# Performance work log

Hardware: AMD Instinct MI355X
Metric: run time of the kernel (lower is better)

Reference implementation:

```python
import jax, jax.numpy as jnp
import numpy as np

K = 3          # kernel size
PAD = 1        # padding


def _conv2d(x, w, b):
    # plain 3x3 conv, stride 1, pad 1, NCHW / OIHW
    out = jax.lax.conv_general_dilated(
        x, w, window_strides=(1, 1), padding=((PAD, PAD), (PAD, PAD)),
        dimension_numbers=('NCHW', 'OIHW', 'NCHW'))
    return out + b[None, :, None, None]


def _deform_conv2d(x, offsets, w, b):
    # torchvision deform_conv2d semantics (stride=1, dilation=1, no mask)
    B, C, H, W = x.shape
    K2 = K * K
    off = offsets.reshape(B, K2, 2, H, W)
    dy, dx = off[:, :, 0], off[:, :, 1]              # [B,K2,H,W], (y,x) order
    ki, kj = jnp.meshgrid(jnp.arange(K), jnp.arange(K), indexing='ij')
    ki = ki.reshape(K2).astype(x.dtype)
    kj = kj.reshape(K2).astype(x.dtype)
    base_y = (jnp.arange(H, dtype=x.dtype)[None, :, None] - PAD + ki[:, None, None])  # [K2,H,1]
    base_x = (jnp.arange(W, dtype=x.dtype)[None, None, :] - PAD + kj[:, None, None])  # [K2,1,W]
    py = base_y[None] + dy                            # [B,K2,H,W] sampling rows
    px = base_x[None] + dx                            # [B,K2,H,W] sampling cols

    y0 = jnp.floor(py); x0 = jnp.floor(px)
    y1 = y0 + 1.0;      x1 = x0 + 1.0
    wy1 = py - y0; wy0 = 1.0 - wy1
    wx1 = px - x0; wx0 = 1.0 - wx1

    def corner(yc, xc, wgt):
        valid = ((yc >= 0) & (yc <= H - 1) & (xc >= 0) & (xc <= W - 1))
        iy = jnp.clip(yc, 0, H - 1).astype(jnp.int32)
        ix = jnp.clip(xc, 0, W - 1).astype(jnp.int32)
        # per-batch gather: x[b][:, iy[b], ix[b]] -> [C,K2,H,W]
        vals = jax.vmap(lambda xb, iyb, ixb: xb[:, iyb, ixb])(x, iy, ix)
        return vals * (wgt * valid.astype(x.dtype))[:, None]  # [B,C,K2,H,W]

    sampled = (corner(y0, x0, wy0 * wx0) + corner(y0, x1, wy0 * wx1)
               + corner(y1, x0, wy1 * wx0) + corner(y1, x1, wy1 * wx1))
    out = jnp.einsum('bckhw,ock->bohw', sampled, w.reshape(w.shape[0], C, K2))
    return out + b[None, :, None, None]


def setup_inputs() -> dict:
    key = jax.random.key(0)
    ks = jax.random.split(key, 6)
    B, C, O, H, W = 4, 256, 256, 64, 64
    x = jax.random.normal(ks[0], (B, C, H, W), dtype=jnp.float32)
    y = jax.random.normal(ks[1], (B, C, H, W), dtype=jnp.float32)
    # offset conv predicts 2*K*K offset channels; small init keeps offsets a few px
    offset_w = jax.random.normal(ks[2], (2 * K * K, C, K, K), dtype=jnp.float32) * 0.01
    offset_b = jax.random.normal(ks[3], (2 * K * K,), dtype=jnp.float32) * 0.01
    deform_w = jax.random.normal(ks[4], (O, C, K, K), dtype=jnp.float32) * (1.0 / np.sqrt(C * K * K))
    deform_b = jax.random.normal(ks[5], (O,), dtype=jnp.float32) * 0.01
    return {"x": x, "y": y, "offset_w": offset_w, "offset_b": offset_b,
            "deform_w": deform_w, "deform_b": deform_b}


def reference(x, y, offset_w, offset_b, deform_w, deform_b):
    offsets = _conv2d(y, offset_w, offset_b)          # [B, 2*K*K, H, W]
    return _deform_conv2d(x, offsets, deform_w, deform_b)
```

## Files before the change

kernel.cpp:

```cpp
#include <hip/hip_runtime.h>
#include <hip/hip_bf16.h>
#include <stdint.h>


typedef __bf16 bf16x8 __attribute__((ext_vector_type(8)));
typedef float  f32x4  __attribute__((ext_vector_type(4)));

__device__ __forceinline__ unsigned short f2bfu(float f) {
    union { float f; unsigned u; } v; v.f = f;
    return (unsigned short)((v.u + 0x8000u) >> 16);
}
__device__ __forceinline__ float lo16(unsigned u) {
    union { unsigned u; float f; } v; v.u = u << 16; return v.f;
}
__device__ __forceinline__ float hi16(unsigned u) {
    union { unsigned u; float f; } v; v.u = u & 0xFFFF0000u; return v.f;
}
__device__ __forceinline__ unsigned fbits(float f) {
    union { float f; unsigned u; } v; v.f = f; return v.u;
}
__device__ __forceinline__ unsigned blend2(unsigned u0, unsigned u1, unsigned u2, unsigned u3,
                                           float4 w) {
    float lo = w.x * lo16(u0) + w.y * lo16(u1) + w.z * lo16(u2) + w.w * lo16(u3);
    float hi = w.x * hi16(u0) + w.y * hi16(u1) + w.z * hi16(u2) + w.w * hi16(u3);
    unsigned rl = fbits(lo) + 0x8000u;
    unsigned rh = fbits(hi) + 0x8000u;
    return __builtin_amdgcn_perm(rh, rl, 0x07060302);
}

__global__ __launch_bounds__(256) void prep_kernel(
    const float* __restrict__ x, const float* __restrict__ y,
    const float* __restrict__ ow, const float* __restrict__ dw,
    unsigned short* __restrict__ xT, unsigned short* __restrict__ yT,
    unsigned short* __restrict__ Wp2, unsigned short* __restrict__ Bo)
{
    __shared__ float tile[64 * 69];
    int blk = blockIdx.x;
    int t = threadIdx.x;
    if (blk < 2048) {
        const float* src = x; unsigned short* dst = xT;
        if (blk >= 1024) { src = y; dst = yT; blk -= 1024; }
        int cq = blk & 3;
        int bh = blk >> 2;
        int w4 = t & 15, cl0 = t >> 4;
        const float* s = src + ((size_t)(bh >> 6) * 256 + cq * 64) * 4096 + (size_t)(bh & 63) * 64;
#pragma unroll
        for (int p = 0; p < 4; ++p) {
            int cl = p * 16 + cl0;
            float4 v = *(const float4*)&s[(size_t)cl * 4096 + w4 * 4];
            tile[(w4 * 4 + 0) * 69 + cl] = v.x;
            tile[(w4 * 4 + 1) * 69 + cl] = v.y;
            tile[(w4 * 4 + 2) * 69 + cl] = v.z;
            tile[(w4 * 4 + 3) * 69 + cl] = v.w;
        }
        __syncthreads();
        unsigned short* d = dst + (size_t)bh * 16384 + cq * 64;
#pragma unroll
        for (int p = 0; p < 4; ++p) {
            int w = p * 16 + cl0;
            float4 v = *(const float4*)&tile[w * 69 + w4 * 4];
            ushort4 r = make_ushort4(f2bfu(v.x), f2bfu(v.y), f2bfu(v.z), f2bfu(v.w));
            *(ushort4*)&d[w * 256 + w4 * 4] = r;
        }
    } else if (blk < 2336) {
        int tid = (blk - 2048) * 256 + t;
        int q8 = tid >> 8;
        int o  = tid & 255;
        int k0 = q8 * 8;
        int tap = k0 >> 8, c0 = k0 & 255;
        const float* s = dw + o * 2304 + c0 * 9 + tap;
        ushort4 r0 = make_ushort4(f2bfu(s[0]), f2bfu(s[9]), f2bfu(s[18]), f2bfu(s[27]));
        ushort4 r1 = make_ushort4(f2bfu(s[36]), f2bfu(s[45]), f2bfu(s[54]), f2bfu(s[63]));
        *(ushort4*)&Wp2[tid * 8 + 0] = r0;
        *(ushort4*)&Wp2[tid * 8 + 4] = r1;
    } else {
        int idx = (blk - 2336) * 256 + t;
        int j = idx & 7;
        int n = (idx >> 3) & 31;
        int lq = (idx >> 8) & 3;
        int kg = idx >> 10;
        int k = kg * 32 + lq * 8 + j;
        int tap = k >> 8, c = k & 255;
        float v = (n < 18) ? ow[n * 2304 + c * 9 + tap] : 0.f;
        Bo[idx] = f2bfu(v);
    }
}

__global__ __launch_bounds__(1024) void deform_kernel(
    const unsigned short* __restrict__ xT,
    const unsigned short* __restrict__ yT,
    const unsigned short* __restrict__ Wp2,
    const unsigned short* __restrict__ Bo,
    const float* __restrict__ ob,
    const float* __restrict__ db,
    float* __restrict__ out)
{
    __shared__ __align__(16) unsigned char smem[88064];
    unsigned short* Abuf0 = (unsigned short*)smem;
    unsigned short* Abuf1 = (unsigned short*)(smem + 32768);
    float*  red = (float*)smem;
    float*  epi = (float*)smem;
    float4* pw_lds = (float4*)(smem + 69632);
    int4*   pi_lds = (int4*)(smem + 69632 + 9216);

    int blk = blockIdx.x;
    int lb = (blk & 7) * 32 + (blk >> 3);
    int b = lb >> 6, h = lb & 63;
    int t = threadIdx.x;
    int wv = t >> 6, lane = t & 63;
    int ln = lane & 15, lq = lane >> 4;

    const unsigned short* xtb = xT + (size_t)b * (64 * 64 * 256);

    {
        int kq = wv >> 1, mh = wv & 1;
        f32x4 oacc[2][2];
#pragma unroll
        for (int m16 = 0; m16 < 2; ++m16)
#pragma unroll
            for (int nt = 0; nt < 2; ++nt)
                oacc[m16][nt] = (f32x4){0.f, 0.f, 0.f, 0.f};
        for (int u = kq * 9; u < kq * 9 + 9; ++u) {
            int tap = u >> 3, kc = u & 7;
            int ki = tap / 3, kj = tap - ki * 3;
            int hr = h + ki - 1;
            bf16x8 b0 = *(const bf16x8*)&Bo[(tap * 8 + kc) * 1024 + lq * 256 + ln * 8];
            bf16x8 b1 = *(const bf16x8*)&Bo[(tap * 8 + kc) * 1024 + lq * 256 + (16 + ln) * 8];
#pragma unroll
            for (int m16 = 0; m16 < 2; ++m16) {
                int wr = mh * 32 + m16 * 16 + ln + kj - 1;
                bf16x8 af = (bf16x8)(__bf16)0.0f;
                if (hr >= 0 && hr < 64 && wr >= 0 && wr < 64)
                    af = *(const bf16x8*)&yT[((size_t)(b * 64 + hr) * 64 + wr) * 256 + kc * 32 + lq * 8];
                oacc[m16][0] = __builtin_amdgcn_mfma_f32_16x16x32_bf16(af, b0, oacc[m16][0], 0, 0, 0);
                oacc[m16][1] = __builtin_amdgcn_mfma_f32_16x16x32_bf16(af, b1, oacc[m16][1], 0, 0, 0);
            }
        }
        float* rz = red + (size_t)(kq * 2 + mh) * 1056;
#pragma unroll
        for (int m16 = 0; m16 < 2; ++m16)
#pragma unroll
            for (int nt = 0; nt < 2; ++nt) {
                int o_l = nt * 16 + ln;
#pragma unroll
                for (int r = 0; r < 4; ++r)
                    rz[o_l * 33 + m16 * 16 + lq * 4 + r] = oacc[m16][nt][r];
            }
    }
    __syncthreads();
    if (t < 576) {
        int tap = t >> 6, pos = t & 63;
        int mh_p = pos >> 5, pl = pos & 31;
        float dy = ob[2 * tap], dx = ob[2 * tap + 1];
#pragma unroll
        for (int kq = 0; kq < 8; ++kq) {
            const float* rz = red + (size_t)(kq * 2 + mh_p) * 1056;
            dy += rz[(2 * tap) * 33 + pl];
            dx += rz[(2 * tap + 1) * 33 + pl];
        }
        int ki = tap / 3, kj = tap - ki * 3;
        float py = (float)(h - 1 + ki) + dy;
        float px = (float)(pos - 1 + kj) + dx;
        float y0 = floorf(py), x0 = floorf(px);
        float wy1 = py - y0, wx1 = px - x0;
        float wy0 = 1.f - wy1, wx0 = 1.f - wx1;
        float y1 = y0 + 1.f, x1 = x0 + 1.f;
        float vy0 = (y0 >= 0.f && y0 <= 63.f) ? 1.f : 0.f;
        float vy1 = (y1 >= 0.f && y1 <= 63.f) ? 1.f : 0.f;
        float vx0 = (x0 >= 0.f && x0 <= 63.f) ? 1.f : 0.f;
        float vx1 = (x1 >= 0.f && x1 <= 63.f) ? 1.f : 0.f;
        int iy0 = (int)fminf(fmaxf(y0, 0.f), 63.f);
        int iy1 = (int)fminf(fmaxf(y1, 0.f), 63.f);
        int ix0 = (int)fminf(fmaxf(x0, 0.f), 63.f);
        int ix1 = (int)fminf(fmaxf(x1, 0.f), 63.f);
        pw_lds[t] = make_float4(wy0 * wx0 * vy0 * vx0, wy0 * wx1 * vy0 * vx1,
                                wy1 * wx0 * vy1 * vx0, wy1 * wx1 * vy1 * vx1);
        pi_lds[t] = make_int4((iy0 * 64 + ix0) * 256, (iy0 * 64 + ix1) * 256,
                              (iy1 * 64 + ix0) * 256, (iy1 * 64 + ix1) * 256);
    }
    __syncthreads();

    int ns = wv & 7, kh = wv >> 3;

    f32x4 acc[4][2];
#pragma unroll
    for (int ms = 0; ms < 4; ++ms)
#pragma unroll
        for (int nt = 0; nt < 2; ++nt)
            acc[ms][nt] = (f32x4){0.f, 0.f, 0.f, 0.f};

    int gr = t & 31, c0 = gr * 8;
    uint4 ga[2][4]; float4 gw[2];
#pragma unroll
    for (int it = 0; it < 2; ++it) {
        int pos = (t >> 5) + it * 32;
        gw[it] = pw_lds[pos];
        int4 p = pi_lds[pos];
        ga[it][0] = *(const uint4*)&xtb[p.x + c0];
        ga[it][1] = *(const uint4*)&xtb[p.y + c0];
        ga[it][2] = *(const uint4*)&xtb[p.z + c0];
        ga[it][3] = *(const uint4*)&xtb[p.w + c0];
    }
#pragma unroll
    for (int it = 0; it < 2; ++it) {
        int pos = (t >> 5) + it * 32;
        uint4 res;
        res.x = blend2(ga[it][0].x, ga[it][1].x, ga[it][2].x, ga[it][3].x, gw[it]);
        res.y = blend2(ga[it][0].y, ga[it][1].y, ga[it][2].y, ga[it][3].y, gw[it]);
        res.z = blend2(ga[it][0].z, ga[it][1].z, ga[it][2].z, ga[it][3].z, gw[it]);
        res.w = blend2(ga[it][0].w, ga[it][1].w, ga[it][2].w, ga[it][3].w, gw[it]);
        *(uint4*)&Abuf0[pos * 256 + (gr ^ (pos & 7)) * 8] = res;
    }
    __syncthreads();

    for (int tap = 0; tap < 9; ++tap) {
        if (tap < 8) {
#pragma unroll
            for (int it = 0; it < 2; ++it) {
                int pos = (t >> 5) + it * 32;
                gw[it] = pw_lds[(tap + 1) * 64 + pos];
                int4 p = pi_lds[(tap + 1) * 64 + pos];
                ga[it][0] = *(const uint4*)&xtb[p.x + c0];
                ga[it][1] = *(const uint4*)&xtb[p.y + c0];
                ga[it][2] = *(const uint4*)&xtb[p.z + c0];
                ga[it][3] = *(const uint4*)&xtb[p.w + c0];
            }
        }
        const unsigned short* Ab = (tap & 1) ? Abuf1 : Abuf0;
#pragma unroll
        for (int kc = 0; kc < 4; ++kc) {
            int gbase = kh * 16 + kc * 4 + lq;
            bf16x8 af[4];
#pragma unroll
            for (int ms = 0; ms < 4; ++ms) {
                int row = ms * 16 + ln;
                af[ms] = *(const bf16x8*)&Ab[row * 256 + (gbase ^ (row & 7)) * 8];
            }
            int kg = tap * 8 + kh * 4 + kc;
            bf16x8 bfr[2];
#pragma unroll
            for (int nt = 0; nt < 2; ++nt)
                bfr[nt] = *(const bf16x8*)&Wp2[((kg * 4 + lq) * 256 + ns * 32 + nt * 16 + ln) * 8];
#pragma unroll
            for (int ms = 0; ms < 4; ++ms)
#pragma unroll
                for (int nt = 0; nt < 2; ++nt)
                    acc[ms][nt] = __builtin_amdgcn_mfma_f32_16x16x32_bf16(af[ms], bfr[nt], acc[ms][nt], 0, 0, 0);
        }
        if (tap < 8) {
            unsigned short* buf = (tap & 1) ? Abuf0 : Abuf1;
#pragma unroll
            for (int it = 0; it < 2; ++it) {
                int pos = (t >> 5) + it * 32;
                uint4 res;
                res.x = blend2(ga[it][0].x, ga[it][1].x, ga[it][2].x, ga[it][3].x, gw[it]);
                res.y = blend2(ga[it][0].y, ga[it][1].y, ga[it][2].y, ga[it][3].y, gw[it]);
                res.z = blend2(ga[it][0].z, ga[it][1].z, ga[it][2].z, ga[it][3].z, gw[it]);
                res.w = blend2(ga[it][0].w, ga[it][1].w, ga[it][2].w, ga[it][3].w, gw[it]);
                *(uint4*)&buf[pos * 256 + (gr ^ (pos & 7)) * 8] = res;
            }
        }
        __syncthreads();
    }

    if (kh == 1) {
        float* e = epi + (size_t)ns * 2176;
#pragma unroll
        for (int ms = 0; ms < 4; ++ms)
#pragma unroll
            for (int nt = 0; nt < 2; ++nt) {
                int o_l = nt * 16 + ln;
                f32x4 a = acc[ms][nt];
                *(float4*)&e[o_l * 68 + ms * 16 + lq * 4] = make_float4(a[0], a[1], a[2], a[3]);
            }
    }
    __syncthreads();
    if (kh == 0) {
        const float* e = epi + (size_t)ns * 2176;
#pragma unroll
        for (int ms = 0; ms < 4; ++ms)
#pragma unroll
            for (int nt = 0; nt < 2; ++nt) {
                int o_l = nt * 16 + ln;
                int o = ns * 32 + o_l;
                float bias = db[o];
                float4 p = *(const float4*)&e[o_l * 68 + ms * 16 + lq * 4];
                f32x4 a = acc[ms][nt];
                float4 st = make_float4(a[0] + p.x + bias, a[1] + p.y + bias,
                                        a[2] + p.z + bias, a[3] + p.w + bias);
                *(float4*)&out[((size_t)(b * 256 + o)) * 4096 + h * 64 + ms * 16 + lq * 4] = st;
            }
    }
}

extern "C" void kernel_launch(void* const* d_in, const int* in_sizes, int n_in,
                              void* d_out, int out_size, void* d_ws, size_t ws_size,
                              hipStream_t stream) {
    const float* x  = (const float*)d_in[0];
    const float* y  = (const float*)d_in[1];
    const float* ow = (const float*)d_in[2];
    const float* ob = (const float*)d_in[3];
    const float* dw = (const float*)d_in[4];
    const float* db = (const float*)d_in[5];
    float* out = (float*)d_out;

    char* ws = (char*)d_ws;
    unsigned short* xT  = (unsigned short*)(ws);
    unsigned short* yT  = (unsigned short*)(ws + 8388608);
    unsigned short* Wp2 = (unsigned short*)(ws + 16777216);
    unsigned short* Bo  = (unsigned short*)(ws + 16777216 + 1179648);

    hipLaunchKernelGGL(prep_kernel, dim3(2624), dim3(256), 0, stream,
                       x, y, ow, dw, xT, yT, Wp2, Bo);
    hipLaunchKernelGGL(deform_kernel, dim3(256), dim3(1024), 0, stream,
                       xT, yT, Wp2, Bo, ob, db, out);
}
```

Measured before the change: 135.2 us.

## Warp-specialize deform kernel into gather producers and MFMA consumers with LDS flags

Splits the 16 waves into 8 producer waves that gather and bilinearly blend sampled rows into a triple-buffered LDS ring, and 8 consumer waves that run the full K=256 MFMA reduction per tap. Per-tap ready/done counters in shared memory replace block-wide barriers. Because each consumer now covers the whole channel range, the cross-wave reduction through LDS in the epilogue goes away. The aim is to overlap gather latency with matrix math. In exchange, LDS use grows to about 114KB and spin-waiting with sleeps adds scheduling risk.

```diff
diff --git a/kernel.cpp b/kernel.cpp
--- a/kernel.cpp
+++ b/kernel.cpp
@@ -26,6 +26,16 @@
     unsigned rl = fbits(lo) + 0x8000u;
     unsigned rh = fbits(hi) + 0x8000u;
     return __builtin_amdgcn_perm(rh, rl, 0x07060302);
+}
+
+__device__ __forceinline__ void wait_ge(int* f, int v) {
+    while (__hip_atomic_load(f, __ATOMIC_ACQUIRE, __HIP_MEMORY_SCOPE_WORKGROUP) < v)
+        __builtin_amdgcn_s_sleep(1);
+}
+__device__ __forceinline__ void signal_one(int* f, int lane) {
+    __threadfence_block();
+    if (lane == 0)
+        __hip_atomic_fetch_add(f, 1, __ATOMIC_RELEASE, __HIP_MEMORY_SCOPE_WORKGROUP);
 }
 
 __global__ __launch_bounds__(256) void prep_kernel(
@@ -95,13 +105,12 @@
     const float* __restrict__ db,
     float* __restrict__ out)
 {
-    __shared__ __align__(16) unsigned char smem[88064];
-    unsigned short* Abuf0 = (unsigned short*)smem;
-    unsigned short* Abuf1 = (unsigned short*)(smem + 32768);
-    float*  red = (float*)smem;
-    float*  epi = (float*)smem;
-    float4* pw_lds = (float4*)(smem + 69632);
-    int4*   pi_lds = (int4*)(smem + 69632 + 9216);
+    __shared__ __align__(16) unsigned char smem[116864];
+    float*  red    = (float*)smem;
+    float4* pw_lds = (float4*)(smem + 98304);
+    int4*   pi_lds = (int4*)(smem + 98304 + 9216);
+    int*    ready  = (int*)(smem + 116736);
+    int*    done   = (int*)(smem + 116736 + 36);
 
     int blk = blockIdx.x;
     int lb = (blk & 7) * 32 + (blk >> 3);
@@ -111,6 +120,8 @@
     int ln = lane & 15, lq = lane >> 4;
 
     const unsigned short* xtb = xT + (size_t)b * (64 * 64 * 256);
+
+    if (t < 18) ((int*)(smem + 116736))[t] = 0;
 
     {
         int kq = wv >> 1, mh = wv & 1;
@@ -180,78 +191,26 @@
     }
     __syncthreads();
 
-    int ns = wv & 7, kh = wv >> 3;
-
-    f32x4 acc[4][2];
-#pragma unroll
-    for (int ms = 0; ms < 4; ++ms)
-#pragma unroll
-        for (int nt = 0; nt < 2; ++nt)
-            acc[ms][nt] = (f32x4){0.f, 0.f, 0.f, 0.f};
-
-    int gr = t & 31, c0 = gr * 8;
-    uint4 ga[2][4]; float4 gw[2];
-#pragma unroll
-    for (int it = 0; it < 2; ++it) {
-        int pos = (t >> 5) + it * 32;
-        gw[it] = pw_lds[pos];
-        int4 p = pi_lds[pos];
-        ga[it][0] = *(const uint4*)&xtb[p.x + c0];
-        ga[it][1] = *(const uint4*)&xtb[p.y + c0];
-        ga[it][2] = *(const uint4*)&xtb[p.z + c0];
-        ga[it][3] = *(const uint4*)&xtb[p.w + c0];
-    }
-#pragma unroll
-    for (int it = 0; it < 2; ++it) {
-        int pos = (t >> 5) + it * 32;
-        uint4 res;
-        res.x = blend2(ga[it][0].x, ga[it][1].x, ga[it][2].x, ga[it][3].x, gw[it]);
-        res.y = blend2(ga[it][0].y, ga[it][1].y, ga[it][2].y, ga[it][3].y, gw[it]);
-        res.z = blend2(ga[it][0].z, ga[it][1].z, ga[it][2].z, ga[it][3].z, gw[it]);
-        res.w = blend2(ga[it][0].w, ga[it][1].w, ga[it][2].w, ga[it][3].w, gw[it]);
-        *(uint4*)&Abuf0[pos * 256 + (gr ^ (pos & 7)) * 8] = res;
-    }
-    __syncthreads();
-
-    for (int tap = 0; tap < 9; ++tap) {
-        if (tap < 8) {
-#pragma unroll
-            for (int it = 0; it < 2; ++it) {
-                int pos = (t >> 5) + it * 32;
-                gw[it] = pw_lds[(tap + 1) * 64 + pos];
-                int4 p = pi_lds[(tap + 1) * 64 + pos];
+    if (wv < 8) {
+        int gr = lane & 31, half = lane >> 5, c0 = gr * 8;
+#pragma unroll 1
+        for (int tap = 0; tap < 9; ++tap) {
+            if (tap >= 3) wait_ge(&done[tap - 3], 8);
+            float4 gw[4]; uint4 ga[4][4];
+#pragma unroll
+            for (int it = 0; it < 4; ++it) {
+                int pos = wv * 2 + half + it * 16;
+                gw[it] = pw_lds[tap * 64 + pos];
+                int4 p = pi_lds[tap * 64 + pos];
                 ga[it][0] = *(const uint4*)&xtb[p.x + c0];
                 ga[it][1] = *(const uint4*)&xtb[p.y + c0];
                 ga[it][2] = *(const uint4*)&xtb[p.z + c0];
                 ga[it][3] = *(const uint4*)&xtb[p.w + c0];
             }
-        }
-        const unsigned short* Ab = (tap & 1) ? Abuf1 : Abuf0;
-#pragma unroll
-        for (int kc = 0; kc < 4; ++kc) {
-            int gbase = kh * 16 + kc * 4 + lq;
-            bf16x8 af[4];
-#pragma unroll
-            for (int ms = 0; ms < 4; ++ms) {
-                int row = ms * 16 + ln;
-                af[ms] = *(const bf16x8*)&Ab[row * 256 + (gbase ^ (row & 7)) * 8];
-            }
-            int kg = tap * 8 + kh * 4 + kc;
-            bf16x8 bfr[2];
-#pragma unroll
-            for (int nt = 0; nt < 2; ++nt)
-                bfr[nt] = *(const bf16x8*)&Wp2[((kg * 4 + lq) * 256 + ns * 32 + nt * 16 + ln) * 8];
-#pragma unroll
-            for (int ms = 0; ms < 4; ++ms)
-#pragma unroll
-                for (int nt = 0; nt < 2; ++nt)
-                    acc[ms][nt] = __builtin_amdgcn_mfma_f32_16x16x32_bf16(af[ms], bfr[nt], acc[ms][nt], 0, 0, 0);
-        }
-        if (tap < 8) {
-            unsigned short* buf = (tap & 1) ? Abuf0 : Abuf1;
-#pragma unroll
-            for (int it = 0; it < 2; ++it) {
-                int pos = (t >> 5) + it * 32;
+            unsigned short* buf = (unsigned short*)(smem + (tap % 3) * 32768);
+#pragma unroll
+            for (int it = 0; it < 4; ++it) {
+                int pos = wv * 2 + half + it * 16;
                 uint4 res;
                 res.x = blend2(ga[it][0].x, ga[it][1].x, ga[it][2].x, ga[it][3].x, gw[it]);
                 res.y = blend2(ga[it][0].y, ga[it][1].y, ga[it][2].y, ga[it][3].y, gw[it]);
@@ -259,37 +218,54 @@
                 res.w = blend2(ga[it][0].w, ga[it][1].w, ga[it][2].w, ga[it][3].w, gw[it]);
                 *(uint4*)&buf[pos * 256 + (gr ^ (pos & 7)) * 8] = res;
             }
-        }
-        __syncthreads();
-    }
-
-    if (kh == 1) {
-        float* e = epi + (size_t)ns * 2176;
+            signal_one(&ready[tap], lane);
+        }
+    } else {
+        int ns = wv - 8;
+        f32x4 acc[4][2];
 #pragma unroll
         for (int ms = 0; ms < 4; ++ms)
 #pragma unroll
-            for (int nt = 0; nt < 2; ++nt) {
-                int o_l = nt * 16 + ln;
+            for (int nt = 0; nt < 2; ++nt)
+                acc[ms][nt] = (f32x4){0.f, 0.f, 0.f, 0.f};
+#pragma unroll 1
+        for (int tap = 0; tap < 9; ++tap) {
+            wait_ge(&ready[tap], 8);
+            const unsigned short* Ab = (const unsigned short*)(smem + (tap % 3) * 32768);
+#pragma unroll 2
+            for (int kc = 0; kc < 8; ++kc) {
+                int g = kc * 4 + lq;
+                bf16x8 af[4];
+#pragma unroll
+                for (int ms = 0; ms < 4; ++ms) {
+                    int row = ms * 16 + ln;
+                    af[ms] = *(const bf16x8*)&Ab[row * 256 + (g ^ (row & 7)) * 8];
+                }
+                int kg = tap * 8 + kc;
+                bf16x8 bfr[2];
+#pragma unroll
+                for (int nt = 0; nt < 2; ++nt)
+                    bfr[nt] = *(const bf16x8*)&Wp2[((kg * 4 + lq) * 256 + ns * 32 + nt * 16 + ln) * 8];
+#pragma unroll
+                for (int ms = 0; ms < 4; ++ms)
+#pragma unroll
+                    for (int nt = 0; nt < 2; ++nt)
+                        acc[ms][nt] = __builtin_amdgcn_mfma_f32_16x16x32_bf16(af[ms], bfr[nt], acc[ms][nt], 0, 0, 0);
+            }
+            signal_one(&done[tap], lane);
+        }
+#pragma unroll
+        for (int nt = 0; nt < 2; ++nt) {
+            int o = ns * 32 + nt * 16 + ln;
+            float bias = db[o];
+            float* ob_ptr = out + ((size_t)(b * 256 + o)) * 4096 + h * 64;
+#pragma unroll
+            for (int ms = 0; ms < 4; ++ms) {
                 f32x4 a = acc[ms][nt];
-                *(float4*)&e[o_l * 68 + ms * 16 + lq * 4] = make_float4(a[0], a[1], a[2], a[3]);
-            }
-    }
-    __syncthreads();
-    if (kh == 0) {
-        const float* e = epi + (size_t)ns * 2176;
-#pragma unroll
-        for (int ms = 0; ms < 4; ++ms)
-#pragma unroll
-            for (int nt = 0; nt < 2; ++nt) {
-                int o_l = nt * 16 + ln;
-                int o = ns * 32 + o_l;
-                float bias = db[o];
-                float4 p = *(const float4*)&e[o_l * 68 + ms * 16 + lq * 4];
-                f32x4 a = acc[ms][nt];
-                float4 st = make_float4(a[0] + p.x + bias, a[1] + p.y + bias,
-                                        a[2] + p.z + bias, a[3] + p.w + bias);
-                *(float4*)&out[((size_t)(b * 256 + o)) * 4096 + h * 64 + ms * 16 + lq * 4] = st;
-            }
+                float4 st = make_float4(a[0] + bias, a[1] + bias, a[2] + bias, a[3] + bias);
+                *(float4*)&ob_ptr[ms * 16 + lq * 4] = st;
+            }
+        }
     }
 }
 
```

After: 137.4 us. Within noise of the previous version (+1.6%).
